# Optimization experiments

Measured on AMD Instinct MI355X. Metric: run time of the kernel, lower is better.

## Reference

```python
import jax, jax.numpy as jnp
import numpy as np

N, E, IN, OUT, H = 100000, 1600000, 128, 128, 4
C = OUT // H
NEG_SLOPE = 0.2  # PyG GATConv default LeakyReLU slope
BN_EPS = 1e-5


def setup_inputs() -> dict:
    key = jax.random.key(0)
    k = jax.random.split(key, 6)
    x = jax.random.normal(k[0], (N, IN), dtype=jnp.float32)
    edge_index = jax.random.randint(k[1], (2, E), 0, N, dtype=jnp.int64)
    W = jax.random.normal(k[2], (IN, H * C), dtype=jnp.float32) / np.sqrt(IN)
    att_src = jax.random.normal(k[3], (H, C), dtype=jnp.float32) * 0.1
    att_dst = jax.random.normal(k[4], (H, C), dtype=jnp.float32) * 0.1
    gat_bias = jnp.zeros((H * C,), dtype=jnp.float32)
    bn_gamma = jnp.ones((OUT,), dtype=jnp.float32)
    bn_beta = jnp.zeros((OUT,), dtype=jnp.float32)
    return {"x": x, "edge_index": edge_index, "W": W, "att_src": att_src,
            "att_dst": att_dst, "gat_bias": gat_bias, "bn_gamma": bn_gamma,
            "bn_beta": bn_beta}


def reference(x, edge_index, W, att_src, att_dst, gat_bias, bn_gamma, bn_beta):
    n = x.shape[0]
    # GATConv: linear transform, per-head view [N,H,C]
    h = (x @ W).reshape(n, H, C)
    # add self loops (PyG default add_self_loops=True)
    loop = jnp.arange(n, dtype=edge_index.dtype)
    src = jnp.concatenate([edge_index[0], loop])  # message source j
    dst = jnp.concatenate([edge_index[1], loop])  # message target i
    # per-node attention logits [N,H]
    a_src = jnp.einsum('nhc,hc->nh', h, att_src)
    a_dst = jnp.einsum('nhc,hc->nh', h, att_dst)
    # per-edge logits [Etot,H], LeakyReLU, segment softmax over dst
    e = jax.nn.leaky_relu(a_src[src] + a_dst[dst], NEG_SLOPE)
    m = jax.ops.segment_max(e, dst, num_segments=n)
    e = jnp.exp(e - m[dst])
    s = jax.ops.segment_sum(e, dst, num_segments=n)
    alpha = e / (s[dst] + 1e-16)  # dropout(p=0.3) is identity at eval
    # weighted scatter-add aggregation
    msg = h[src] * alpha[:, :, None]  # [Etot,H,C]
    out = jax.ops.segment_sum(msg, dst, num_segments=n).reshape(n, H * C)
    out = out + gat_bias
    # BatchNorm1d (batch statistics, biased var)
    mean = jnp.mean(out, axis=0)
    var = jnp.var(out, axis=0)
    out = bn_gamma * (out - mean) * jax.lax.rsqrt(var + BN_EPS) + bn_beta
    # residual (proj is Identity since in_ch == out_ch) + ReLU
    return jax.nn.relu(out + x)
```

## Files before the change

kernel.cpp:

```cpp
#include <hip/hip_runtime.h>

#define NEG 0.2f
#define EPB 8192
#define NB64MAX 1568
#define CAPB_MAX 1536
#define REPL 16

typedef short short8 __attribute__((ext_vector_type(8)));
typedef float floatx4 __attribute__((ext_vector_type(4)));

__device__ __forceinline__ float bf_lo(unsigned int u) { return __uint_as_float(u << 16); }
__device__ __forceinline__ float bf_hi(unsigned int u) { return __uint_as_float(u & 0xffff0000u); }
__device__ __forceinline__ unsigned short f2bf(float f) {
    unsigned int u = __float_as_uint(f);
    return (unsigned short)((u + 0x7fff + ((u >> 16) & 1)) >> 16);
}

__global__ __launch_bounds__(256) void k_wconv(const float* __restrict__ W,
                                               unsigned short* __restrict__ Wtb,
                                               int* __restrict__ gcur,
                                               float* __restrict__ gsum,
                                               float* __restrict__ gsumsq, int NB) {
    int i = blockIdx.x * 256 + threadIdx.x;
    int n = i >> 7, k = i & 127;
    Wtb[n * 128 + k] = f2bf(W[k * 128 + n]);
    if (i < NB) gcur[i] = 0;
    if (i < REPL * 128) { gsum[i] = 0.f; gsumsq[i] = 0.f; }
}

__global__ __launch_bounds__(256) void k_gemm(const float* __restrict__ x,
                                              const unsigned short* __restrict__ Wtb,
                                              const float* __restrict__ att_src,
                                              const float* __restrict__ att_dst,
                                              unsigned short* __restrict__ hb,
                                              unsigned int* __restrict__ asd, int N) {
    __shared__ unsigned short As[64 * 128];
    __shared__ unsigned short Bs[128 * 128];
    int t = threadIdx.x;
    int r0 = blockIdx.x * 64;
#pragma unroll
    for (int p = 0; p < 8; p++) {
        int idx = t + 256 * p;
        int row = idx >> 5, c4 = idx & 31;
        float4 v = make_float4(0.f, 0.f, 0.f, 0.f);
        if (r0 + row < N) v = *(const float4*)&x[(size_t)(r0 + row) * 128 + c4 * 4];
        int kb = c4 >> 1;
        uint2* d = (uint2*)&As[row * 128 + ((kb ^ (row & 7)) << 3) + (c4 & 1) * 4];
        uint2 pk;
        pk.x = ((unsigned int)f2bf(v.y) << 16) | f2bf(v.x);
        pk.y = ((unsigned int)f2bf(v.w) << 16) | f2bf(v.z);
        *d = pk;
    }
#pragma unroll
    for (int p = 0; p < 8; p++) {
        int idx = t + 256 * p;
        int n = idx >> 4, k8 = idx & 15;
        *(short8*)&Bs[n * 128 + ((k8 ^ (n & 7)) << 3)] = *(const short8*)&Wtb[n * 128 + k8 * 8];
    }
    __syncthreads();
    int lane = t & 63, wv = t >> 6;
    int m16 = lane & 15, quad = lane >> 4;
    int rowbase = wv * 16;
    floatx4 acc[8];
#pragma unroll
    for (int c = 0; c < 8; c++) acc[c] = (floatx4){0.f, 0.f, 0.f, 0.f};
#pragma unroll
    for (int ks = 0; ks < 4; ks++) {
        int arow = rowbase + m16;
        short8 a = *(const short8*)&As[arow * 128 + (((ks * 4 + quad) ^ (arow & 7)) << 3)];
#pragma unroll
        for (int c = 0; c < 8; c++) {
            int brow = c * 16 + m16;
            short8 b = *(const short8*)&Bs[brow * 128 + (((ks * 4 + quad) ^ (brow & 7)) << 3)];
            acc[c] = __builtin_amdgcn_mfma_f32_16x16x32_bf16(a, b, acc[c], 0, 0, 0);
        }
    }
    float ps[4][4], pd[4][4];
#pragma unroll
    for (int hd = 0; hd < 4; hd++)
#pragma unroll
        for (int r = 0; r < 4; r++) { ps[hd][r] = 0.f; pd[hd][r] = 0.f; }
#pragma unroll
    for (int c = 0; c < 8; c++) {
        int col = c * 16 + m16;
        float as_ = att_src[col], ad_ = att_dst[col];
        int hd = c >> 1;
#pragma unroll
        for (int r = 0; r < 4; r++) {
            float v = acc[c][r];
            int row = r0 + rowbase + quad * 4 + r;
            if (row < N) hb[(size_t)row * 128 + col] = f2bf(v);
            ps[hd][r] = fmaf(v, as_, ps[hd][r]);
            pd[hd][r] = fmaf(v, ad_, pd[hd][r]);
        }
    }
#pragma unroll
    for (int off = 1; off < 16; off <<= 1) {
#pragma unroll
        for (int hd = 0; hd < 4; hd++)
#pragma unroll
            for (int r = 0; r < 4; r++) {
                ps[hd][r] += __shfl_xor(ps[hd][r], off, 16);
                pd[hd][r] += __shfl_xor(pd[hd][r], off, 16);
            }
    }
    if (m16 == 0) {
#pragma unroll
        for (int r = 0; r < 4; r++) {
            int row = r0 + rowbase + quad * 4 + r;
            if (row < N)
#pragma unroll
                for (int hd = 0; hd < 4; hd++)
                    asd[row * 4 + hd] = ((unsigned int)f2bf(pd[hd][r]) << 16) | f2bf(ps[hd][r]);
        }
    }
}

__global__ __launch_bounds__(512) void k_bin3(const int* __restrict__ ei,
                                              int* __restrict__ gcur,
                                              unsigned int* __restrict__ pairs,
                                              int E, int NB, int CAPB) {
    __shared__ int cnt[NB64MAX];
    __shared__ int lbase[NB64MAX];
    int t = threadIdx.x;
    for (int i = t; i < NB; i += 512) cnt[i] = 0;
    __syncthreads();
    int base = blockIdx.x * EPB, end = min(base + EPB, E);
    for (int i = base + t; i < end; i += 512) atomicAdd(&cnt[ei[E + i] >> 6], 1);
    __syncthreads();
    for (int i = t; i < NB; i += 512) {
        int c = cnt[i];
        if (c) {
            int s = atomicAdd(&gcur[i], c);
            lbase[i] = (s + c <= CAPB) ? s : -1;
        }
    }
    __syncthreads();
    for (int i = base + t; i < end; i += 512) {
        int d = ei[E + i];
        int b = d >> 6;
        int lb = lbase[b];
        if (lb >= 0) {
            int slot = atomicSub(&cnt[b], 1) - 1;
            pairs[(size_t)b * CAPB + lb + slot] =
                (unsigned int)ei[i] | ((unsigned int)(d & 63) << 20);
        }
    }
}

__global__ __launch_bounds__(256) void k_agg2(const unsigned int* __restrict__ hb,
                                              const unsigned int* __restrict__ asd,
                                              const int* __restrict__ gcur,
                                              const unsigned int* __restrict__ pairs,
                                              unsigned int* __restrict__ yb,
                                              float* __restrict__ gsum,
                                              float* __restrict__ gsumsq,
                                              int N, int CAPB) {
    __shared__ unsigned int ent[CAPB_MAX];
    __shared__ float red[1024];
    __shared__ int cnt64[64], off64[64], cur64[64], stmp[64];
    int b = blockIdx.x, t = threadIdx.x;
    size_t base = (size_t)b * CAPB;
    int cnt = min(gcur[b], CAPB);
    if (t < 64) cnt64[t] = 0;
    __syncthreads();
    unsigned int pe[6];
#pragma unroll
    for (int q = 0; q < 6; q++) {
        int i = t + q * 256;
        unsigned int e = 0xFFFFFFFFu;
        if (i < cnt) {
            e = pairs[base + i];
            atomicAdd(&cnt64[(e >> 20) & 63], 1);
        }
        pe[q] = e;
    }
    __syncthreads();
    if (t < 64) stmp[t] = cnt64[t];
    __syncthreads();
    for (int d = 1; d < 64; d <<= 1) {
        int add = (t < 64 && t >= d) ? stmp[t - d] : 0;
        __syncthreads();
        if (t < 64) stmp[t] += add;
        __syncthreads();
    }
    if (t < 64) { int ex = stmp[t] - cnt64[t]; off64[t] = ex; cur64[t] = ex; }
    __syncthreads();
#pragma unroll
    for (int q = 0; q < 6; q++) {
        unsigned int e = pe[q];
        if (e != 0xFFFFFFFFu) {
            int slot = atomicAdd(&cur64[(e >> 20) & 63], 1);
            ent[slot] = e & 0xFFFFFu;
        }
    }
    __syncthreads();
    int lane = t & 63, wv = t >> 6;
    int head = lane >> 4, sub = lane & 15, wsel = lane & 48;
    float t_sl = 0.f, t_sh = 0.f, t_ql = 0.f, t_qh = 0.f;
    for (int k = 0; k < 16; k++) {
        int ln = wv * 16 + k;
        int n = b * 64 + ln;
        if (n >= N) break;
        unsigned int au = asd[n * 4 + head];
        float adst = bf_hi(au);
        float e0 = bf_lo(au) + adst;
        e0 = e0 > 0.f ? e0 : NEG * e0;
        float w0 = __expf(e0);
        unsigned int hu = hb[(size_t)n * 64 + lane];
        float acc0 = w0 * bf_lo(hu), acc1 = w0 * bf_hi(hu), sw = w0;
        int st = off64[ln], c = cnt64[ln];
        int sjn = n;
        float evn = 0.f;
        if (sub < c) {
            sjn = (int)ent[st + sub];
            evn = bf_lo(asd[sjn * 4 + head]);
        }
        for (int eb = 0; eb < c; eb += 16) {
            int sj_l = sjn;
            float ev = evn + adst;
            ev = ev > 0.f ? ev : NEG * ev;
            float wl = (eb + sub < c) ? __expf(ev) : 0.f;
            if (eb + 16 + sub < c) {
                sjn = (int)ent[st + eb + 16 + sub];
                evn = bf_lo(asd[sjn * 4 + head]);
            } else sjn = n;
#pragma unroll
            for (int j = 0; j < 16; j++) {
                int sj = __shfl(sj_l, j, 64);
                float wj = __shfl(wl, wsel | j, 64);
                unsigned int hj = hb[(size_t)sj * 64 + lane];
                acc0 = fmaf(wj, bf_lo(hj), acc0);
                acc1 = fmaf(wj, bf_hi(hj), acc1);
                sw += wj;
            }
        }
        float inv = 1.0f / (sw + 1e-16f);
        unsigned int yw = ((unsigned int)f2bf(acc1 * inv) << 16) | f2bf(acc0 * inv);
        yb[(size_t)n * 64 + lane] = yw;
        float ylo = bf_lo(yw), yhi = bf_hi(yw);
        t_sl += ylo; t_sh += yhi;
        t_ql = fmaf(ylo, ylo, t_ql);
        t_qh = fmaf(yhi, yhi, t_qh);
    }
    red[t] = t_sl; red[256 + t] = t_sh; red[512 + t] = t_ql; red[768 + t] = t_qh;
    __syncthreads();
    if (t < 64) {
        float a = red[t] + red[t + 64] + red[t + 128] + red[t + 192];
        float bb = red[256 + t] + red[256 + t + 64] + red[256 + t + 128] + red[256 + t + 192];
        float cc = red[512 + t] + red[512 + t + 64] + red[512 + t + 128] + red[512 + t + 192];
        float dd = red[768 + t] + red[768 + t + 64] + red[768 + t + 128] + red[768 + t + 192];
        int rep = (b & (REPL - 1)) * 128;
        atomicAdd(&gsum[rep + 2 * t], a);
        atomicAdd(&gsum[rep + 2 * t + 1], bb);
        atomicAdd(&gsumsq[rep + 2 * t], cc);
        atomicAdd(&gsumsq[rep + 2 * t + 1], dd);
    }
}

__global__ __launch_bounds__(256) void k_final(const unsigned int* __restrict__ yb,
                                               const float* __restrict__ x,
                                               const float* __restrict__ gsum,
                                               const float* __restrict__ gsumsq,
                                               const float* __restrict__ gamma,
                                               const float* __restrict__ beta,
                                               float* __restrict__ out, int N, int total4) {
    __shared__ float scS[128], shS[128];
    int t = threadIdx.x;
    if (t < 128) {
        float s = 0.f, q = 0.f;
#pragma unroll
        for (int r = 0; r < REPL; r++) {
            s += gsum[r * 128 + t];
            q += gsumsq[r * 128 + t];
        }
        float invN = 1.0f / (float)N;
        float mean = s * invN;
        float var = q * invN - mean * mean;
        float sc = gamma[t] * rsqrtf(var + 1e-5f);
        scS[t] = sc;
        shS[t] = beta[t] - mean * sc;
    }
    __syncthreads();
    int i = blockIdx.x * 256 + t;
    if (i >= total4) return;
    int c4 = i & 31;
    uint2 u = ((const uint2*)yb)[i];
    float4 xv = ((const float4*)x)[i];
    float4 r;
    r.x = fmaxf(fmaf(bf_lo(u.x), scS[c4 * 4 + 0], shS[c4 * 4 + 0]) + xv.x, 0.f);
    r.y = fmaxf(fmaf(bf_hi(u.x), scS[c4 * 4 + 1], shS[c4 * 4 + 1]) + xv.y, 0.f);
    r.z = fmaxf(fmaf(bf_lo(u.y), scS[c4 * 4 + 2], shS[c4 * 4 + 2]) + xv.z, 0.f);
    r.w = fmaxf(fmaf(bf_hi(u.y), scS[c4 * 4 + 3], shS[c4 * 4 + 3]) + xv.w, 0.f);
    ((float4*)out)[i] = r;
}

extern "C" void kernel_launch(void* const* d_in, const int* in_sizes, int n_in,
                              void* d_out, int out_size, void* d_ws, size_t ws_size,
                              hipStream_t stream) {
    const float* x       = (const float*)d_in[0];
    const int*   ei      = (const int*)d_in[1];
    const float* W       = (const float*)d_in[2];
    const float* att_src = (const float*)d_in[3];
    const float* att_dst = (const float*)d_in[4];
    const float* gamma   = (const float*)d_in[6];
    const float* beta    = (const float*)d_in[7];
    int N = in_sizes[0] / 128;
    int E = in_sizes[1] / 2;
    int NB = (N + 63) / 64;

    char* base = (char*)d_ws;
    size_t off = 0;
    auto alloc = [&](size_t b) -> char* {
        char* p = base + off;
        off = (off + b + 255) & ~(size_t)255;
        return p;
    };
    unsigned short* hb  = (unsigned short*)alloc((size_t)N * 128 * 2);
    unsigned int*   yb  = (unsigned int*)alloc((size_t)N * 64 * 4);
    unsigned int*   asd = (unsigned int*)alloc((size_t)N * 4 * 4);
    unsigned short* Wtb = (unsigned short*)alloc(128 * 128 * 2);
    int*   gcur   = (int*)alloc((size_t)NB * 4);
    float* gsum   = (float*)alloc(REPL * 128 * 4);
    float* gsumsq = (float*)alloc(REPL * 128 * 4);
    size_t rem = (ws_size > off) ? (ws_size - off) : 0;
    int CAPB = (int)((rem / ((size_t)NB * 4)) & ~(size_t)15);
    if (CAPB > CAPB_MAX) CAPB = CAPB_MAX;
    unsigned int* pairs = (unsigned int*)alloc((size_t)NB * CAPB * 4);
    float* outp = (float*)d_out;

    int chunks = (E + EPB - 1) / EPB;
    k_wconv<<<64, 256, 0, stream>>>(W, Wtb, gcur, gsum, gsumsq, NB);
    k_gemm<<<(N + 63) / 64, 256, 0, stream>>>(x, Wtb, att_src, att_dst, hb, asd, N);
    k_bin3<<<chunks, 512, 0, stream>>>(ei, gcur, pairs, E, NB, CAPB);
    k_agg2<<<NB, 256, 0, stream>>>((const unsigned int*)hb, asd, gcur, pairs, yb,
                                   gsum, gsumsq, N, CAPB);
    k_final<<<(N * 32 + 255) / 256, 256, 0, stream>>>(yb, x, gsum, gsumsq, gamma, beta,
                                                      outp, N, N * 32);
}
```

Baseline: 282.8 us.

## Reduce atomic contention in binning and BN stats; hoist BN finalize into own kernel

Halves edges per binning block and rotates the order in which each block claims per-bucket global cursors, spreading atomic contention on gcur. Increases the number of replicated BN-statistic accumulators to cut atomic collisions in the aggregation kernel. Moves the mean/variance/scale computation into a single tiny kernel so each final elementwise block only loads 256 precomputed floats instead of re-reducing all replicas. Adds an extra kernel launch and relies on the init kernel zeroing the larger replica buffers.

Result: slower. 290.9 us (+2.9%).

```diff
diff --git a/kernel.cpp b/kernel.cpp
--- a/kernel.cpp
+++ b/kernel.cpp
@@ -1,10 +1,10 @@
 #include <hip/hip_runtime.h>
 
 #define NEG 0.2f
-#define EPB 8192
+#define EPB 4096
 #define NB64MAX 1568
 #define CAPB_MAX 1536
-#define REPL 16
+#define REPL 64
 
 typedef short short8 __attribute__((ext_vector_type(8)));
 typedef float floatx4 __attribute__((ext_vector_type(4)));
@@ -128,7 +128,10 @@
     int base = blockIdx.x * EPB, end = min(base + EPB, E);
     for (int i = base + t; i < end; i += 512) atomicAdd(&cnt[ei[E + i] >> 6], 1);
     __syncthreads();
-    for (int i = t; i < NB; i += 512) {
+    int rot = (int)((blockIdx.x * 401u) % (unsigned)NB);
+    for (int ii = t; ii < NB; ii += 512) {
+        int i = ii + rot;
+        if (i >= NB) i -= NB;
         int c = cnt[i];
         if (c) {
             int s = atomicAdd(&gcur[i], c);
@@ -258,29 +261,35 @@
     }
 }
 
+__global__ __launch_bounds__(128) void k_bnfinal(const float* __restrict__ gsum,
+                                                 const float* __restrict__ gsumsq,
+                                                 const float* __restrict__ gamma,
+                                                 const float* __restrict__ beta,
+                                                 float* __restrict__ scale,
+                                                 float* __restrict__ shift, int N) {
+    int c = threadIdx.x;
+    float s = 0.f, q = 0.f;
+#pragma unroll
+    for (int r = 0; r < REPL; r++) {
+        s += gsum[r * 128 + c];
+        q += gsumsq[r * 128 + c];
+    }
+    float invN = 1.0f / (float)N;
+    float mean = s * invN;
+    float var = q * invN - mean * mean;
+    float sc = gamma[c] * rsqrtf(var + 1e-5f);
+    scale[c] = sc;
+    shift[c] = beta[c] - mean * sc;
+}
+
 __global__ __launch_bounds__(256) void k_final(const unsigned int* __restrict__ yb,
                                                const float* __restrict__ x,
-                                               const float* __restrict__ gsum,
-                                               const float* __restrict__ gsumsq,
-                                               const float* __restrict__ gamma,
-                                               const float* __restrict__ beta,
-                                               float* __restrict__ out, int N, int total4) {
+                                               const float* __restrict__ scale,
+                                               const float* __restrict__ shift,
+                                               float* __restrict__ out, int total4) {
     __shared__ float scS[128], shS[128];
     int t = threadIdx.x;
-    if (t < 128) {
-        float s = 0.f, q = 0.f;
-#pragma unroll
-        for (int r = 0; r < REPL; r++) {
-            s += gsum[r * 128 + t];
-            q += gsumsq[r * 128 + t];
-        }
-        float invN = 1.0f / (float)N;
-        float mean = s * invN;
-        float var = q * invN - mean * mean;
-        float sc = gamma[t] * rsqrtf(var + 1e-5f);
-        scS[t] = sc;
-        shS[t] = beta[t] - mean * sc;
-    }
+    if (t < 128) { scS[t] = scale[t]; shS[t] = shift[t]; }
     __syncthreads();
     int i = blockIdx.x * 256 + t;
     if (i >= total4) return;
@@ -323,6 +332,8 @@
     int*   gcur   = (int*)alloc((size_t)NB * 4);
     float* gsum   = (float*)alloc(REPL * 128 * 4);
     float* gsumsq = (float*)alloc(REPL * 128 * 4);
+    float* scale  = (float*)alloc(512);
+    float* shift  = (float*)alloc(512);
     size_t rem = (ws_size > off) ? (ws_size - off) : 0;
     int CAPB = (int)((rem / ((size_t)NB * 4)) & ~(size_t)15);
     if (CAPB > CAPB_MAX) CAPB = CAPB_MAX;
@@ -335,6 +346,6 @@
     k_bin3<<<chunks, 512, 0, stream>>>(ei, gcur, pairs, E, NB, CAPB);
     k_agg2<<<NB, 256, 0, stream>>>((const unsigned int*)hb, asd, gcur, pairs, yb,
                                    gsum, gsumsq, N, CAPB);
-    k_final<<<(N * 32 + 255) / 256, 256, 0, stream>>>(yb, x, gsum, gsumsq, gamma, beta,
-                                                      outp, N, N * 32);
-}
+    k_bnfinal<<<1, 128, 0, stream>>>(gsum, gsumsq, gamma, beta, scale, shift, N);
+    k_final<<<(N * 32 + 255) / 256, 256, 0, stream>>>(yb, x, scale, shift, outp, N * 32);
+}
```

## Sort edges by bucket in LDS before coalesced writes in k_bin3

Applied to the files above, without the earlier changes.

The binning kernel now loads each block's edges into registers once, counts per-bucket, runs a block-wide prefix scan, and places the edges into a bucket-sorted staging array in shared memory. It then writes pairs out in sorted order, so consecutive threads write contiguous global addresses instead of scattered ones. This removes the second global read of the edge list and is meant to make the scattered pair stores coalesced. In exchange it uses about 48KB more shared memory per block, which can reduce occupancy, and it adds extra barriers and a scan.

After: 278.2 us. Within noise of the previous version (-1.6%).

```diff
diff --git a/kernel.cpp b/kernel.cpp
--- a/kernel.cpp
+++ b/kernel.cpp
@@ -120,31 +120,87 @@
                                               int* __restrict__ gcur,
                                               unsigned int* __restrict__ pairs,
                                               int E, int NB, int CAPB) {
+    __shared__ unsigned int sorted[EPB];
+    __shared__ unsigned short bkt[EPB];
     __shared__ int cnt[NB64MAX];
-    __shared__ int lbase[NB64MAX];
+    __shared__ int A[NB64MAX];
+    __shared__ int wsum[8];
     int t = threadIdx.x;
     for (int i = t; i < NB; i += 512) cnt[i] = 0;
     __syncthreads();
     int base = blockIdx.x * EPB, end = min(base + EPB, E);
-    for (int i = base + t; i < end; i += 512) atomicAdd(&cnt[ei[E + i] >> 6], 1);
-    __syncthreads();
-    for (int i = t; i < NB; i += 512) {
-        int c = cnt[i];
-        if (c) {
-            int s = atomicAdd(&gcur[i], c);
-            lbase[i] = (s + c <= CAPB) ? s : -1;
-        }
-    }
-    __syncthreads();
-    for (int i = base + t; i < end; i += 512) {
-        int d = ei[E + i];
-        int b = d >> 6;
-        int lb = lbase[b];
-        if (lb >= 0) {
-            int slot = atomicSub(&cnt[b], 1) - 1;
-            pairs[(size_t)b * CAPB + lb + slot] =
-                (unsigned int)ei[i] | ((unsigned int)(d & 63) << 20);
-        }
+    int nLoc = end - base;
+    unsigned int pay[16];
+    unsigned short bk[16];
+#pragma unroll
+    for (int q = 0; q < 16; q++) {
+        int i = base + t + q * 512;
+        unsigned int p = 0xFFFFFFFFu;
+        int b = 0;
+        if (i < end) {
+            int s = ei[i], d = ei[E + i];
+            p = (unsigned int)s | ((unsigned int)(d & 63) << 20);
+            b = d >> 6;
+            atomicAdd(&cnt[b], 1);
+        }
+        pay[q] = p;
+        bk[q] = (unsigned short)b;
+    }
+    __syncthreads();
+    int b0 = 4 * t;
+    int c0 = 0, c1 = 0, c2 = 0, c3 = 0;
+    if (b0 < NB)     c0 = cnt[b0];
+    if (b0 + 1 < NB) c1 = cnt[b0 + 1];
+    if (b0 + 2 < NB) c2 = cnt[b0 + 2];
+    if (b0 + 3 < NB) c3 = cnt[b0 + 3];
+    int local = c0 + c1 + c2 + c3;
+    int lane = t & 63, wv = t >> 6;
+    int scan = local;
+#pragma unroll
+    for (int off = 1; off < 64; off <<= 1) {
+        int v = __shfl_up(scan, off, 64);
+        if (lane >= off) scan += v;
+    }
+    if (lane == 63) wsum[wv] = scan;
+    __syncthreads();
+    int woff = 0;
+    for (int w = 0; w < wv; w++) woff += wsum[w];
+    int lst = woff + scan - local;
+    if (b0 < NB) {
+        int s = c0 ? atomicAdd(&gcur[b0], c0) : 0;
+        A[b0] = (s + c0 <= CAPB) ? (b0 * CAPB + s - lst) : INT_MIN;
+        cnt[b0] = lst + c0; lst += c0;
+    }
+    if (b0 + 1 < NB) {
+        int s = c1 ? atomicAdd(&gcur[b0 + 1], c1) : 0;
+        A[b0 + 1] = (s + c1 <= CAPB) ? ((b0 + 1) * CAPB + s - lst) : INT_MIN;
+        cnt[b0 + 1] = lst + c1; lst += c1;
+    }
+    if (b0 + 2 < NB) {
+        int s = c2 ? atomicAdd(&gcur[b0 + 2], c2) : 0;
+        A[b0 + 2] = (s + c2 <= CAPB) ? ((b0 + 2) * CAPB + s - lst) : INT_MIN;
+        cnt[b0 + 2] = lst + c2; lst += c2;
+    }
+    if (b0 + 3 < NB) {
+        int s = c3 ? atomicAdd(&gcur[b0 + 3], c3) : 0;
+        A[b0 + 3] = (s + c3 <= CAPB) ? ((b0 + 3) * CAPB + s - lst) : INT_MIN;
+        cnt[b0 + 3] = lst + c3;
+    }
+    __syncthreads();
+#pragma unroll
+    for (int q = 0; q < 16; q++) {
+        if (pay[q] != 0xFFFFFFFFu) {
+            int b = bk[q];
+            int pos = atomicSub(&cnt[b], 1) - 1;
+            sorted[pos] = pay[q];
+            bkt[pos] = (unsigned short)b;
+        }
+    }
+    __syncthreads();
+    for (int i = t; i < nLoc; i += 512) {
+        int b = bkt[i];
+        int a = A[b];
+        if (a != INT_MIN) pairs[(size_t)(a + i)] = sorted[i];
     }
 }
 
```
